# Performance work log

Hardware: AMD Instinct MI355X
Metric: run time of the kernel (lower is better)

## Reference

```python
import jax, jax.numpy as jnp
import numpy as np

B, S, D, H = 2, 2048, 1024, 16
DK = D // H


def setup_inputs() -> dict:
    key = jax.random.key(0)
    ks = jax.random.split(key, 12)
    s = 0.02
    return {
        "q": jax.random.normal(ks[0], (B, S, D), jnp.float32),
        "k": jax.random.normal(ks[1], (B, S, D), jnp.float32),
        "v": jax.random.normal(ks[2], (B, S, D), jnp.float32),
        "mask": jax.random.randint(ks[3], (1, 1, S, S), 0, 2, jnp.int32),
        "Wq": jax.random.normal(ks[4], (D, D), jnp.float32) * s,
        "bq": jnp.zeros((D,), jnp.float32),
        "Wk": jax.random.normal(ks[5], (D, D), jnp.float32) * s,
        "bk": jnp.zeros((D,), jnp.float32),
        "Wv": jax.random.normal(ks[6], (D, D), jnp.float32) * s,
        "bv": jnp.zeros((D,), jnp.float32),
        "Wo": jax.random.normal(ks[7], (D, D), jnp.float32) * s,
        "bo": jnp.zeros((D,), jnp.float32),
    }


def reference(q, k, v, mask, Wq, bq, Wk, bk, Wv, bv, Wo, bo):
    # linear projections (torch Linear: x @ W.T + b)
    qp = q @ Wq.T + bq
    kp = k @ Wk.T + bk
    vp = v @ Wv.T + bv
    # [B, S, D] -> [B, H, S, DK]
    split = lambda x: x.reshape(B, S, H, DK).transpose(0, 2, 1, 3)
    qh, kh, vh = split(qp), split(kp), split(vp)
    scale = 1.0 / jnp.sqrt(jnp.float32(DK))
    attn = jnp.einsum('bhsd,bhtd->bhst', qh, kh) * scale  # [B,H,S,S]
    attn = jnp.where(mask == 0, jnp.float32(-1e9), attn)
    attn = jax.nn.softmax(attn, axis=-1)
    out = jnp.einsum('bhst,bhtd->bhsd', attn, vh)  # [B,H,S,DK]
    concat = out.transpose(0, 2, 1, 3).reshape(B, S, D)
    return concat @ Wo.T + bo
```

## Files before the change

kernel.cpp:

```cpp
#include <hip/hip_runtime.h>
#include <hip/hip_bf16.h>


using bf16x8 = __attribute__((ext_vector_type(8))) short;
using f32x4  = __attribute__((ext_vector_type(4))) float;
using f32x16 = __attribute__((ext_vector_type(16))) float;

constexpr int Bc = 2, Sc = 2048, Dc = 1024, Hc = 16, DKc = 64;
constexpr int Mc = Bc * Sc;
#define QSCALE 0.18033688011112042f

__device__ __forceinline__ void lds_load16(const void* g, void* l) {
  __builtin_amdgcn_global_load_lds(
      (const __attribute__((address_space(1))) unsigned int*)g,
      (__attribute__((address_space(3))) unsigned int*)l, 16, 0, 0);
}

#if __has_builtin(__builtin_amdgcn_exp2f)
__device__ __forceinline__ float exp2_fast(float x) { return __builtin_amdgcn_exp2f(x); }
#else
__device__ __forceinline__ float exp2_fast(float x) {
  float r;
  asm("v_exp_f32 %0, %1\n\ts_nop 0" : "=v"(r) : "v"(x));
  return r;
}
#endif

__device__ __forceinline__ unsigned cvt_pk_bf16(float lo, float hi) {
  unsigned r;
  asm("v_cvt_pk_bf16_f32 %0, %1, %2" : "=v"(r) : "v"(lo), "v"(hi));
  return r;
}

#define PSWAP(A, B) \
  asm volatile("v_permlane32_swap_b32 %0, %1" : "+v"(A), "+v"(B))

__device__ __forceinline__ unsigned pack2bf(float a, float b) {
  union { __hip_bfloat16 h; unsigned short s; } ua, ub;
  ua.h = __float2bfloat16(a);
  ub.h = __float2bfloat16(b);
  return (unsigned)ua.s | ((unsigned)ub.s << 16);
}

__global__ void prep(const float* __restrict__ q, const float* __restrict__ k,
                     const float* __restrict__ v, const int* __restrict__ mask,
                     const float* __restrict__ Wq, const float* __restrict__ Wk,
                     const float* __restrict__ Wv, const float* __restrict__ Wo,
                     char* __restrict__ ws) {
  const size_t MB = 1024 * 1024;
  int blk = blockIdx.x;
  int tid = threadIdx.x;
  if (blk < 6144) {
    int which = blk >> 11;
    int i = (((blk & 2047) << 8) + tid) * 8;
    const float* s = which == 0 ? q : (which == 1 ? k : v);
    __hip_bfloat16* d = (__hip_bfloat16*)(ws + (size_t)which * 8 * MB);
    float4 x = *(const float4*)&s[i];
    float4 y = *(const float4*)&s[i + 4];
    uint4 pk = {pack2bf(x.x, x.y), pack2bf(x.z, x.w),
                pack2bf(y.x, y.y), pack2bf(y.z, y.w)};
    *(uint4*)&d[i] = pk;
  } else if (blk < 8192) {
    int bb = blk - 6144;
    int which = bb >> 9;
    int i = (((bb & 511) << 8) + tid) * 8;
    const float* s = which == 0 ? Wq : (which == 1 ? Wk : (which == 2 ? Wv : Wo));
    __hip_bfloat16* d = which < 3 ? (__hip_bfloat16*)(ws + (24 + 2 * which) * MB)
                                  : (__hip_bfloat16*)(ws + 30 * MB);
    float4 x = *(const float4*)&s[i];
    float4 y = *(const float4*)&s[i + 4];
    uint4 pk = {pack2bf(x.x, x.y), pack2bf(x.z, x.w),
                pack2bf(y.x, y.y), pack2bf(y.z, y.w)};
    *(uint4*)&d[i] = pk;
  } else {
    int blkm = blk - 8192;
    int i0 = ((blkm << 8) + tid) * 4;
    uint4 m = *(const uint4*)&mask[i0];
    unsigned nib = (m.x != 0 ? 1u : 0u) | (m.y != 0 ? 2u : 0u) |
                   (m.z != 0 ? 4u : 0u) | (m.w != 0 ? 8u : 0u);
    unsigned long long w = (unsigned long long)nib << (4 * (tid & 15));
    w |= __shfl_xor(w, 1);
    w |= __shfl_xor(w, 2);
    w |= __shfl_xor(w, 4);
    w |= __shfl_xor(w, 8);
    if ((tid & 15) == 0)
      ((unsigned long long*)(ws + 32 * MB))[(blkm << 4) + (tid >> 4)] = w;
  }
}

__global__ __launch_bounds__(256, 3) void proj_qkv(
    const __hip_bfloat16* __restrict__ qb, const __hip_bfloat16* __restrict__ kb,
    const __hip_bfloat16* __restrict__ vb, const __hip_bfloat16* __restrict__ Wcat,
    const float* __restrict__ bq, const float* __restrict__ bk,
    const float* __restrict__ bv, __hip_bfloat16* __restrict__ qhd,
    __hip_bfloat16* __restrict__ khd, __hip_bfloat16* __restrict__ vtd) {
  __shared__ __align__(16) __hip_bfloat16 As[2][128 * 32];
  __shared__ __align__(16) __hip_bfloat16 Bs[2][128 * 32];
  const int tid = threadIdx.x;
  const int f = blockIdx.x, g = f >> 3;
  const int m0 = ((f & 7) * 4 + g / 24) * 128;
  const int n0 = (g % 24) * 128;
  const int which = n0 >> 10, nl0 = n0 & 1023;
  const __hip_bfloat16* X = which == 0 ? qb : (which == 1 ? kb : vb);
  const float* bias = which == 0 ? bq : (which == 1 ? bk : bv);
  const int w = tid >> 6, lane = tid & 63, ln = lane & 15, quad = lane >> 4;
  const int rl = w * 32 + (lane >> 2);
  const int sw8 = ((lane & 3) ^ ((lane >> 2) & 3)) * 8;
  const int aoff = (n0 + rl) * 1024 + sw8;
  const int boff = (m0 + rl) * 1024 + sw8;
  char* aDst = (char*)As + w * 2048 + lane * 16;
  char* bDst = (char*)Bs + w * 2048 + lane * 16;
  const int rkq = (quad ^ (ln & 3)) * 16;
  const int rA0 = ((w >> 1) * 64 + ln) * 64 + rkq;
  const int rB0 = ((w & 1) * 64 + ln) * 64 + rkq;
  f32x4 acc[4][4] = {};

#define PSTAGE(KO, BI)                                                        \
  {                                                                           \
    lds_load16(&Wcat[aoff + (KO)], aDst + (BI)*8192);                         \
    lds_load16(&Wcat[aoff + 16384 + (KO)], aDst + (BI)*8192 + 1024);          \
    lds_load16(&X[boff + (KO)], bDst + (BI)*8192);                            \
    lds_load16(&X[boff + 16384 + (KO)], bDst + (BI)*8192 + 1024);             \
  }

  PSTAGE(0, 0);
  if (which == 2) {
    for (int kb32 = 0; kb32 < 32; ++kb32) {
      const int bi = kb32 & 1;
      __syncthreads();
      if (kb32 < 31) PSTAGE((kb32 + 1) * 32, bi ^ 1);
      bf16x8 af[4], bf[4];
#pragma unroll
      for (int i = 0; i < 4; ++i)
        af[i] = *(bf16x8*)((char*)As + bi * 8192 + rA0 + i * 1024);
#pragma unroll
      for (int j = 0; j < 4; ++j)
        bf[j] = *(bf16x8*)((char*)Bs + bi * 8192 + rB0 + j * 1024);
#pragma unroll
      for (int i = 0; i < 4; ++i)
#pragma unroll
        for (int j = 0; j < 4; ++j)
          acc[i][j] = __builtin_amdgcn_mfma_f32_16x16x32_bf16(bf[j], af[i],
                                                              acc[i][j], 0, 0, 0);
    }
  } else {
    for (int kb32 = 0; kb32 < 32; ++kb32) {
      const int bi = kb32 & 1;
      __syncthreads();
      if (kb32 < 31) PSTAGE((kb32 + 1) * 32, bi ^ 1);
      bf16x8 af[4], bf[4];
#pragma unroll
      for (int i = 0; i < 4; ++i)
        af[i] = *(bf16x8*)((char*)As + bi * 8192 + rA0 + i * 1024);
#pragma unroll
      for (int j = 0; j < 4; ++j)
        bf[j] = *(bf16x8*)((char*)Bs + bi * 8192 + rB0 + j * 1024);
#pragma unroll
      for (int i = 0; i < 4; ++i)
#pragma unroll
        for (int j = 0; j < 4; ++j)
          acc[i][j] = __builtin_amdgcn_mfma_f32_16x16x32_bf16(af[i], bf[j],
                                                              acc[i][j], 0, 0, 0);
    }
  }

  const int wA = (w >> 1) * 64, wB = (w & 1) * 64;
  if (which == 2) {
#pragma unroll
    for (int i = 0; i < 4; ++i) {
      int nf = nl0 + wA + i * 16 + ln;
      int h = nf >> 6, dk = nf & 63;
      float bb = bias[nf];
#pragma unroll
      for (int j = 0; j < 4; ++j) {
        int sb = m0 + wB + j * 16 + quad * 4;
        int b = sb >> 11, s = sb & 2047;
        float vv[4] = {acc[i][j][0] + bb, acc[i][j][1] + bb,
                       acc[i][j][2] + bb, acc[i][j][3] + bb};
        uint2 pk = {pack2bf(vv[0], vv[1]), pack2bf(vv[2], vv[3])};
        *(uint2*)&vtd[(((size_t)(b * Hc + h) * DKc + dk) * Sc) + s] = pk;
      }
    }
  } else {
#pragma unroll
    for (int i = 0; i < 4; ++i) {
      int nfb = nl0 + wA + i * 16 + quad * 4;
      float4 b4 = *(const float4*)&bias[nfb];
      int h = nfb >> 6, dk0 = nfb & 63;
#pragma unroll
      for (int j = 0; j < 4; ++j) {
        int sg = m0 + wB + j * 16 + ln;
        int b = sg >> 11, s = sg & 2047;
        float vv[4] = {acc[i][j][0] + b4.x, acc[i][j][1] + b4.y,
                       acc[i][j][2] + b4.z, acc[i][j][3] + b4.w};
        if (which == 0) {
          uint2 pk = {pack2bf(vv[0] * QSCALE, vv[1] * QSCALE),
                      pack2bf(vv[2] * QSCALE, vv[3] * QSCALE)};
          *(uint2*)&qhd[(((size_t)(b * Hc + h) * Sc + s) * DKc) + dk0] = pk;
        } else {
          uint2 pk = {pack2bf(vv[0], vv[1]), pack2bf(vv[2], vv[3])};
          *(uint2*)&khd[(((size_t)(b * Hc + h) * Sc + s) * DKc) + dk0] = pk;
        }
      }
    }
  }
}

__global__ __launch_bounds__(256, 2) void gemm_out(
    const __hip_bfloat16* __restrict__ X, const __hip_bfloat16* __restrict__ W,
    const float* __restrict__ bias, float* __restrict__ Y) {
  __shared__ __align__(16) __hip_bfloat16 As[2][64 * 64];
  __shared__ __align__(16) __hip_bfloat16 Bs[2][128 * 64];
  const int tid = threadIdx.x;
  const int f = blockIdx.x, g = f >> 3;
  const int m0 = ((f & 7) * 4 + (g >> 4)) * 128;
  const int n0 = (g & 15) * 64;
  const int w = tid >> 6, lane = tid & 63, ln = lane & 15, quad = lane >> 4;
  const int wA = (w & 1) * 32, wB = (w >> 1) * 64;
  const int swz = ((lane & 7) ^ (lane >> 3)) * 8;
  const int rk0 = ln * 128 + ((quad ^ (ln & 7)) * 16);
  const int rk1 = ln * 128 + (((quad + 4) ^ (ln & 7)) * 16);
  const int aoff = (n0 + w * 16 + (lane >> 3)) * 1024 + swz;
  const int boff = (m0 + w * 32 + (lane >> 3)) * 1024 + swz;
  f32x4 acc[2][4] = {};

#define OSTAGE(KO, BI)                                                        \
  {                                                                           \
    _Pragma("unroll") for (int i = 0; i < 2; ++i)                             \
        lds_load16(&W[aoff + i * 8192 + (KO)],                                \
                   (char*)As[BI] + w * 2048 + lane * 16 + i * 1024);          \
    _Pragma("unroll") for (int i = 0; i < 4; ++i)                             \
        lds_load16(&X[boff + i * 8192 + (KO)],                                \
                   (char*)Bs[BI] + w * 4096 + lane * 16 + i * 1024);          \
  }

  OSTAGE(0, 0);
  for (int kb64 = 0; kb64 < 16; ++kb64) {
    const int bi = kb64 & 1;
    __syncthreads();
    if (kb64 + 1 < 16) OSTAGE((kb64 + 1) * 64, bi ^ 1);
    bf16x8 af[2][2], bf[4][2];
#pragma unroll
    for (int i = 0; i < 2; ++i) {
      af[i][0] = *(bf16x8*)((char*)As[bi] + wA * 128 + i * 2048 + rk0);
      af[i][1] = *(bf16x8*)((char*)As[bi] + wA * 128 + i * 2048 + rk1);
    }
#pragma unroll
    for (int j = 0; j < 4; ++j) {
      bf[j][0] = *(bf16x8*)((char*)Bs[bi] + wB * 128 + j * 2048 + rk0);
      bf[j][1] = *(bf16x8*)((char*)Bs[bi] + wB * 128 + j * 2048 + rk1);
    }
#pragma unroll
    for (int i = 0; i < 2; ++i)
#pragma unroll
      for (int j = 0; j < 4; ++j) {
        acc[i][j] = __builtin_amdgcn_mfma_f32_16x16x32_bf16(af[i][0], bf[j][0],
                                                            acc[i][j], 0, 0, 0);
        acc[i][j] = __builtin_amdgcn_mfma_f32_16x16x32_bf16(af[i][1], bf[j][1],
                                                            acc[i][j], 0, 0, 0);
      }
  }
#pragma unroll
  for (int i = 0; i < 2; ++i) {
    int nfb = n0 + wA + i * 16 + quad * 4;
    float4 b4 = *(const float4*)&bias[nfb];
#pragma unroll
    for (int j = 0; j < 4; ++j) {
      int sg = m0 + wB + j * 16 + ln;
      float4 st = {acc[i][j][0] + b4.x, acc[i][j][1] + b4.y,
                   acc[i][j][2] + b4.z, acc[i][j][3] + b4.w};
      *(float4*)&Y[(size_t)sg * Dc + nfb] = st;
    }
  }
}

__global__ __launch_bounds__(256, 2) void flash_attn(
    const __hip_bfloat16* __restrict__ qh, const __hip_bfloat16* __restrict__ kh,
    const __hip_bfloat16* __restrict__ vt, const uint2* __restrict__ mb2,
    __hip_bfloat16* __restrict__ oc) {
  __shared__ __align__(16) char L[32768];
  const int tid = threadIdx.x;
  const int f = blockIdx.x, g = f >> 3;
  const int bh = (f & 7) * 4 + (g >> 4);
  const int q0 = (g & 15) * 128;
  const int b = bh >> 4, h = bh & 15;
  const int w = tid >> 6, lane = tid & 63, l31 = lane & 31, hi = lane >> 5;
  const size_t base = (size_t)bh * Sc * DKc;
  const __hip_bfloat16* khb = kh + base;
  const __hip_bfloat16* vtb = vt + base;
  const int qglob = q0 + w * 32 + l31;

  bf16x8 qf[4];
#pragma unroll
  for (int dt = 0; dt < 4; ++dt)
    qf[dt] = *(const bf16x8*)&qh[base + (size_t)qglob * 64 + dt * 16 + hi * 8];

  bf16x8 onesA;
#pragma unroll
  for (int i = 0; i < 8; ++i) onesA[i] = (short)0x3F80;

  const int trow = tid >> 3, tcol = tid & 7;
  const int kbase = trow * 64 + ((tcol ^ (trow & 7)) * 8);
  const int vbase = trow * 2048 + ((tcol ^ (trow & 7)) * 8);
  char* Ld = L + tid * 16;

  const int rowb = l31 * 128;
  const int xs = lane & 7;

  f32x16 Oacc0 = {}, Oacc1 = {}, lacc = {};

#define STAGE(BI, T)                                                          \
  {                                                                           \
    lds_load16(khb + kbase + (T)*4096,        Ld + (BI)*8192);                \
    lds_load16(khb + kbase + (T)*4096 + 2048, Ld + (BI)*8192 + 4096);         \
    lds_load16(vtb + vbase + (T)*64,          Ld + 16384 + (BI)*8192);        \
    lds_load16(vtb + vbase + (T)*64 + 65536,  Ld + 16384 + (BI)*8192 + 4096); \
  }

#define PROC_SUB(BOFF, SUB, MW)                                               \
  {                                                                           \
    bf16x8 kf0 = *(bf16x8*)(L + (BOFF) + (SUB)*4096 + rowb + (((0 + hi) ^ xs) * 16)); \
    bf16x8 kf1 = *(bf16x8*)(L + (BOFF) + (SUB)*4096 + rowb + (((2 + hi) ^ xs) * 16)); \
    bf16x8 kf2 = *(bf16x8*)(L + (BOFF) + (SUB)*4096 + rowb + (((4 + hi) ^ xs) * 16)); \
    bf16x8 kf3 = *(bf16x8*)(L + (BOFF) + (SUB)*4096 + rowb + (((6 + hi) ^ xs) * 16)); \
    f32x16 c = {};                                                            \
    __builtin_amdgcn_s_setprio(1);                                            \
    c = __builtin_amdgcn_mfma_f32_32x32x16_bf16(kf0, qf[0], c, 0, 0, 0);      \
    c = __builtin_amdgcn_mfma_f32_32x32x16_bf16(kf1, qf[1], c, 0, 0, 0);      \
    c = __builtin_amdgcn_mfma_f32_32x32x16_bf16(kf2, qf[2], c, 0, 0, 0);      \
    c = __builtin_amdgcn_mfma_f32_32x32x16_bf16(kf3, qf[3], c, 0, 0, 0);      \
    __builtin_amdgcn_s_setprio(0);                                            \
    unsigned shm = (MW) >> (hi * 4);                                          \
    float p[16];                                                              \
    _Pragma("unroll") for (int r = 0; r < 16; ++r) {                          \
      unsigned tg = shm >> (8 * (r >> 2));                                    \
      float e = exp2_fast(c[r]);                                              \
      p[r] = (tg & (1u << (r & 3))) ? e : 0.f;                                \
    }                                                                         \
    unsigned w0 = cvt_pk_bf16(p[0], p[1]),   w1 = cvt_pk_bf16(p[2], p[3]);    \
    unsigned w2 = cvt_pk_bf16(p[4], p[5]),   w3 = cvt_pk_bf16(p[6], p[7]);    \
    unsigned w4 = cvt_pk_bf16(p[8], p[9]),   w5 = cvt_pk_bf16(p[10], p[11]);  \
    unsigned w6 = cvt_pk_bf16(p[12], p[13]), w7 = cvt_pk_bf16(p[14], p[15]);  \
    PSWAP(w0, w2); PSWAP(w1, w3); PSWAP(w4, w6); PSWAP(w5, w7);               \
    { union { unsigned u[4]; bf16x8 v; } t;                                   \
      t.u[0] = w0; t.u[1] = w1; t.u[2] = w2; t.u[3] = w3;                     \
      pb[(SUB)*2] = t.v; }                                                    \
    { union { unsigned u[4]; bf16x8 v; } t;                                   \
      t.u[0] = w4; t.u[1] = w5; t.u[2] = w6; t.u[3] = w7;                     \
      pb[(SUB)*2 + 1] = t.v; }                                                \
  }

  const uint2* mrow = mb2 + (size_t)qglob * 32;
  uint2 mbC = mrow[0];
  STAGE(0, 0);

  for (int t = 0; t < 32; ++t) {
    __syncthreads();
    uint2 mbN = mbC;
    if (t < 31) {
      mbN = mrow[t + 1];
      STAGE((t + 1) & 1, t + 1);
    }
    const int boff = (t & 1) * 8192;

    bf16x8 pb[4];
    PROC_SUB(boff, 0, mbC.x);
    PROC_SUB(boff, 1, mbC.y);

    __builtin_amdgcn_s_setprio(1);
#pragma unroll
    for (int kt = 0; kt < 4; ++kt) {
      lacc = __builtin_amdgcn_mfma_f32_32x32x16_bf16(onesA, pb[kt], lacc, 0, 0, 0);
      bf16x8 vf0 = *(bf16x8*)(L + 16384 + boff + rowb + (((kt * 2 + hi) ^ xs) * 16));
      bf16x8 vf1 = *(bf16x8*)(L + 16384 + boff + 4096 + rowb + (((kt * 2 + hi) ^ xs) * 16));
      Oacc0 = __builtin_amdgcn_mfma_f32_32x32x16_bf16(vf0, pb[kt], Oacc0, 0, 0, 0);
      Oacc1 = __builtin_amdgcn_mfma_f32_32x32x16_bf16(vf1, pb[kt], Oacc1, 0, 0, 0);
    }
    __builtin_amdgcn_s_setprio(0);
    mbC = mbN;
  }

  float linv = 1.f / fmaxf(lacc[0], 1e-30f);
  const size_t obase = (size_t)(b * Sc + qglob) * Dc + h * 64;
#pragma unroll
  for (int gq = 0; gq < 4; ++gq) {
    int d0 = gq * 8 + hi * 4;
    uint2 pk0 = {pack2bf(Oacc0[4 * gq] * linv, Oacc0[4 * gq + 1] * linv),
                 pack2bf(Oacc0[4 * gq + 2] * linv, Oacc0[4 * gq + 3] * linv)};
    *(uint2*)&oc[obase + d0] = pk0;
    uint2 pk1 = {pack2bf(Oacc1[4 * gq] * linv, Oacc1[4 * gq + 1] * linv),
                 pack2bf(Oacc1[4 * gq + 2] * linv, Oacc1[4 * gq + 3] * linv)};
    *(uint2*)&oc[obase + 32 + d0] = pk1;
  }
#undef STAGE
#undef PROC_SUB
}

extern "C" void kernel_launch(void* const* d_in, const int* in_sizes, int n_in,
                              void* d_out, int out_size, void* d_ws, size_t ws_size,
                              hipStream_t stream) {
  const float* q  = (const float*)d_in[0];
  const float* k  = (const float*)d_in[1];
  const float* v  = (const float*)d_in[2];
  const int* mask = (const int*)d_in[3];
  const float* Wq = (const float*)d_in[4];
  const float* bq = (const float*)d_in[5];
  const float* Wk = (const float*)d_in[6];
  const float* bk = (const float*)d_in[7];
  const float* Wv = (const float*)d_in[8];
  const float* bv = (const float*)d_in[9];
  const float* Wo = (const float*)d_in[10];
  const float* bo = (const float*)d_in[11];

  char* ws = (char*)d_ws;
  const size_t MB = 1024 * 1024;
  __hip_bfloat16* qb   = (__hip_bfloat16*)(ws + 0 * MB);
  __hip_bfloat16* kb   = (__hip_bfloat16*)(ws + 8 * MB);
  __hip_bfloat16* vb   = (__hip_bfloat16*)(ws + 16 * MB);
  __hip_bfloat16* Wcat = (__hip_bfloat16*)(ws + 24 * MB);
  __hip_bfloat16* Wob  = (__hip_bfloat16*)(ws + 30 * MB);
  uint2*          mb2  = (uint2*)(ws + 32 * MB);
  __hip_bfloat16* qhd  = (__hip_bfloat16*)(ws + 33 * MB);
  __hip_bfloat16* khd  = (__hip_bfloat16*)(ws + 41 * MB);
  __hip_bfloat16* vtd  = (__hip_bfloat16*)(ws + 49 * MB);
  __hip_bfloat16* oc   = (__hip_bfloat16*)(ws + 57 * MB);

  prep<<<12288, 256, 0, stream>>>(q, k, v, mask, Wq, Wk, Wv, Wo, ws);
  proj_qkv<<<768, 256, 0, stream>>>(qb, kb, vb, Wcat, bq, bk, bv, qhd, khd, vtd);
  flash_attn<<<512, 256, 0, stream>>>(qhd, khd, vtd, mb2, oc);
  gemm_out<<<512, 256, 0, stream>>>(oc, Wob, bo, (float*)d_out);
}
```

Baseline: 238.5 us.

## Software-pipeline attention loop: overlap QK^T of next tile with PV of previous

Restructures the flash attention inner loop so each iteration issues the QK^T MFMAs for the current KV tile, then the PV MFMAs for the previous tile, then the exp/mask softmax work. LDS goes from double to triple buffering (48KB) so the previous tile's V stays resident while the next tile loads. The intent is to hide the exp/convert VALU latency behind independent MFMA work. The cost is higher LDS use per block, which may lower occupancy (launch bounds still ask for 2 blocks), and more live registers.

```diff
diff --git a/kernel.cpp b/kernel.cpp
--- a/kernel.cpp
+++ b/kernel.cpp
@@ -278,7 +278,7 @@
     const __hip_bfloat16* __restrict__ qh, const __hip_bfloat16* __restrict__ kh,
     const __hip_bfloat16* __restrict__ vt, const uint2* __restrict__ mb2,
     __hip_bfloat16* __restrict__ oc) {
-  __shared__ __align__(16) char L[32768];
+  __shared__ __align__(16) char L[49152];
   const int tid = threadIdx.x;
   const int f = blockIdx.x, g = f >> 3;
   const int bh = (f & 7) * 4 + (g >> 4);
@@ -308,33 +308,37 @@
   const int xs = lane & 7;
 
   f32x16 Oacc0 = {}, Oacc1 = {}, lacc = {};
-
-#define STAGE(BI, T)                                                          \
-  {                                                                           \
-    lds_load16(khb + kbase + (T)*4096,        Ld + (BI)*8192);                \
-    lds_load16(khb + kbase + (T)*4096 + 2048, Ld + (BI)*8192 + 4096);         \
-    lds_load16(vtb + vbase + (T)*64,          Ld + 16384 + (BI)*8192);        \
-    lds_load16(vtb + vbase + (T)*64 + 65536,  Ld + 16384 + (BI)*8192 + 4096); \
-  }
-
-#define PROC_SUB(BOFF, SUB, MW)                                               \
+  bf16x8 pbC[4];
+  f32x16 cA, cB;
+
+#define STAGE_OFF(BOFF, T)                                                    \
+  {                                                                           \
+    lds_load16(khb + kbase + (T)*4096,        Ld + (BOFF));                   \
+    lds_load16(khb + kbase + (T)*4096 + 2048, Ld + (BOFF) + 4096);            \
+    lds_load16(vtb + vbase + (T)*64,          Ld + 24576 + (BOFF));           \
+    lds_load16(vtb + vbase + (T)*64 + 65536,  Ld + 24576 + (BOFF) + 4096);    \
+  }
+
+#define QKT_SUB(BOFF, SUB, CV)                                                \
   {                                                                           \
     bf16x8 kf0 = *(bf16x8*)(L + (BOFF) + (SUB)*4096 + rowb + (((0 + hi) ^ xs) * 16)); \
     bf16x8 kf1 = *(bf16x8*)(L + (BOFF) + (SUB)*4096 + rowb + (((2 + hi) ^ xs) * 16)); \
     bf16x8 kf2 = *(bf16x8*)(L + (BOFF) + (SUB)*4096 + rowb + (((4 + hi) ^ xs) * 16)); \
     bf16x8 kf3 = *(bf16x8*)(L + (BOFF) + (SUB)*4096 + rowb + (((6 + hi) ^ xs) * 16)); \
-    f32x16 c = {};                                                            \
-    __builtin_amdgcn_s_setprio(1);                                            \
-    c = __builtin_amdgcn_mfma_f32_32x32x16_bf16(kf0, qf[0], c, 0, 0, 0);      \
-    c = __builtin_amdgcn_mfma_f32_32x32x16_bf16(kf1, qf[1], c, 0, 0, 0);      \
-    c = __builtin_amdgcn_mfma_f32_32x32x16_bf16(kf2, qf[2], c, 0, 0, 0);      \
-    c = __builtin_amdgcn_mfma_f32_32x32x16_bf16(kf3, qf[3], c, 0, 0, 0);      \
-    __builtin_amdgcn_s_setprio(0);                                            \
+    f32x16 zz_ = {};                                                          \
+    CV = __builtin_amdgcn_mfma_f32_32x32x16_bf16(kf0, qf[0], zz_, 0, 0, 0);   \
+    CV = __builtin_amdgcn_mfma_f32_32x32x16_bf16(kf1, qf[1], CV, 0, 0, 0);    \
+    CV = __builtin_amdgcn_mfma_f32_32x32x16_bf16(kf2, qf[2], CV, 0, 0, 0);    \
+    CV = __builtin_amdgcn_mfma_f32_32x32x16_bf16(kf3, qf[3], CV, 0, 0, 0);    \
+  }
+
+#define SM_SUB(CV, MW, PB0, PB1)                                              \
+  {                                                                           \
     unsigned shm = (MW) >> (hi * 4);                                          \
     float p[16];                                                              \
     _Pragma("unroll") for (int r = 0; r < 16; ++r) {                          \
       unsigned tg = shm >> (8 * (r >> 2));                                    \
-      float e = exp2_fast(c[r]);                                              \
+      float e = exp2_fast(CV[r]);                                             \
       p[r] = (tg & (1u << (r & 3))) ? e : 0.f;                                \
     }                                                                         \
     unsigned w0 = cvt_pk_bf16(p[0], p[1]),   w1 = cvt_pk_bf16(p[2], p[3]);    \
@@ -342,43 +346,61 @@
     unsigned w4 = cvt_pk_bf16(p[8], p[9]),   w5 = cvt_pk_bf16(p[10], p[11]);  \
     unsigned w6 = cvt_pk_bf16(p[12], p[13]), w7 = cvt_pk_bf16(p[14], p[15]);  \
     PSWAP(w0, w2); PSWAP(w1, w3); PSWAP(w4, w6); PSWAP(w5, w7);               \
-    { union { unsigned u[4]; bf16x8 v; } t;                                   \
-      t.u[0] = w0; t.u[1] = w1; t.u[2] = w2; t.u[3] = w3;                     \
-      pb[(SUB)*2] = t.v; }                                                    \
-    { union { unsigned u[4]; bf16x8 v; } t;                                   \
-      t.u[0] = w4; t.u[1] = w5; t.u[2] = w6; t.u[3] = w7;                     \
-      pb[(SUB)*2 + 1] = t.v; }                                                \
+    { union { unsigned u[4]; bf16x8 v; } tt_;                                 \
+      tt_.u[0] = w0; tt_.u[1] = w1; tt_.u[2] = w2; tt_.u[3] = w3;             \
+      PB0 = tt_.v; }                                                          \
+    { union { unsigned u[4]; bf16x8 v; } tt_;                                 \
+      tt_.u[0] = w4; tt_.u[1] = w5; tt_.u[2] = w6; tt_.u[3] = w7;             \
+      PB1 = tt_.v; }                                                          \
+  }
+
+#define PV_CLUSTER(VOFF)                                                      \
+  {                                                                           \
+    __builtin_amdgcn_s_setprio(1);                                            \
+    _Pragma("unroll") for (int kt = 0; kt < 4; ++kt) {                        \
+      bf16x8 vf0 = *(bf16x8*)(L + 24576 + (VOFF) + rowb + (((kt * 2 + hi) ^ xs) * 16)); \
+      bf16x8 vf1 = *(bf16x8*)(L + 24576 + (VOFF) + 4096 + rowb + (((kt * 2 + hi) ^ xs) * 16)); \
+      lacc  = __builtin_amdgcn_mfma_f32_32x32x16_bf16(onesA, pbC[kt], lacc, 0, 0, 0); \
+      Oacc0 = __builtin_amdgcn_mfma_f32_32x32x16_bf16(vf0, pbC[kt], Oacc0, 0, 0, 0);  \
+      Oacc1 = __builtin_amdgcn_mfma_f32_32x32x16_bf16(vf1, pbC[kt], Oacc1, 0, 0, 0);  \
+    }                                                                         \
+    __builtin_amdgcn_s_setprio(0);                                            \
   }
 
   const uint2* mrow = mb2 + (size_t)qglob * 32;
   uint2 mbC = mrow[0];
-  STAGE(0, 0);
-
-  for (int t = 0; t < 32; ++t) {
+  STAGE_OFF(0, 0);
+  __syncthreads();
+  uint2 mbN = mrow[1];
+  STAGE_OFF(8192, 1);
+  __builtin_amdgcn_s_setprio(1);
+  QKT_SUB(0, 0, cA);
+  QKT_SUB(0, 1, cB);
+  __builtin_amdgcn_s_setprio(0);
+  SM_SUB(cA, mbC.x, pbC[0], pbC[1]);
+  SM_SUB(cB, mbC.y, pbC[2], pbC[3]);
+  mbC = mbN;
+
+  int curo = 8192, prevo = 0;
+  for (int t = 1; t < 32; ++t) {
     __syncthreads();
-    uint2 mbN = mbC;
     if (t < 31) {
       mbN = mrow[t + 1];
-      STAGE((t + 1) & 1, t + 1);
-    }
-    const int boff = (t & 1) * 8192;
-
-    bf16x8 pb[4];
-    PROC_SUB(boff, 0, mbC.x);
-    PROC_SUB(boff, 1, mbC.y);
-
+      int nxto = curo + 8192; if (nxto == 24576) nxto = 0;
+      STAGE_OFF(nxto, t + 1);
+    }
     __builtin_amdgcn_s_setprio(1);
-#pragma unroll
-    for (int kt = 0; kt < 4; ++kt) {
-      lacc = __builtin_amdgcn_mfma_f32_32x32x16_bf16(onesA, pb[kt], lacc, 0, 0, 0);
-      bf16x8 vf0 = *(bf16x8*)(L + 16384 + boff + rowb + (((kt * 2 + hi) ^ xs) * 16));
-      bf16x8 vf1 = *(bf16x8*)(L + 16384 + boff + 4096 + rowb + (((kt * 2 + hi) ^ xs) * 16));
-      Oacc0 = __builtin_amdgcn_mfma_f32_32x32x16_bf16(vf0, pb[kt], Oacc0, 0, 0, 0);
-      Oacc1 = __builtin_amdgcn_mfma_f32_32x32x16_bf16(vf1, pb[kt], Oacc1, 0, 0, 0);
-    }
+    QKT_SUB(curo, 0, cA);
+    QKT_SUB(curo, 1, cB);
     __builtin_amdgcn_s_setprio(0);
+    PV_CLUSTER(prevo);
+    SM_SUB(cA, mbC.x, pbC[0], pbC[1]);
+    SM_SUB(cB, mbC.y, pbC[2], pbC[3]);
+    prevo = curo;
+    curo += 8192; if (curo == 24576) curo = 0;
     mbC = mbN;
   }
+  PV_CLUSTER(prevo);
 
   float linv = 1.f / fmaxf(lacc[0], 1e-30f);
   const size_t obase = (size_t)(b * Sc + qglob) * Dc + h * 64;
@@ -392,8 +414,10 @@
                  pack2bf(Oacc1[4 * gq + 2] * linv, Oacc1[4 * gq + 3] * linv)};
     *(uint2*)&oc[obase + 32 + d0] = pk1;
   }
-#undef STAGE
-#undef PROC_SUB
+#undef STAGE_OFF
+#undef QKT_SUB
+#undef SM_SUB
+#undef PV_CLUSTER
 }
 
 extern "C" void kernel_launch(void* const* d_in, const int* in_sizes, int n_in,
```

New measurement: 238.8 us (median of 2 runs). Within noise of the previous version (+0.1%).
